# Kernel optimization log

Measured on AMD Instinct MI355X. Metric: run time of the kernel, lower is better.

The kernel has to match this reference:

```python
import jax, jax.numpy as jnp
import numpy as np

TOPK = 8            # args.topk
SWAP_RATIO = 0.3    # args.swap_ratio
NUM_SPECIAL = 999   # first non-special wordpiece id in bert-base-uncased


def setup_inputs() -> dict:
    key = jax.random.key(0)
    k0, k1, k2, k3, k4, k5 = jax.random.split(key, 6)
    B, S, V, D = 4, 512, 30522, 768
    return {
        "delta_grad": jax.random.normal(k0, (B, S, D), jnp.float32),
        "src_embeds": jax.random.normal(k1, (B, S, D), jnp.float32),
        "embedding_matrix": jax.random.normal(k2, (V, D), jnp.float32),
        "src_tokens": jax.random.randint(k3, (B, S), 0, V),
        "pred_lm": jax.random.normal(k4, (B, S, V), jnp.float32),
        "attention_mask": jnp.ones((B, S), jnp.int32),
        "rand_u": jax.random.uniform(k5, (B, S), jnp.float32),
    }


def reference(delta_grad, src_embeds, embedding_matrix, src_tokens, pred_lm, attention_mask, rand_u):
    B, S, D = delta_grad.shape
    V = embedding_matrix.shape[0]
    neg_inf = jnp.float32(-np.inf)

    # dir_dot_grad = -(prev_dot - new_dot) = new_dot - prev_dot
    new_dot = jnp.einsum('bsd,vd->bsv', delta_grad, embedding_matrix)   # [B,S,V]
    prev_dot = jnp.einsum('bsd,bsd->bs', delta_grad, src_embeds)        # [B,S]
    dir_dot_grad = new_dot - prev_dot[..., None]

    # pairwise euclidean distance between src_embeds and vocab embeddings
    src_sq = jnp.sum(src_embeds * src_embeds, axis=-1)                  # [B,S]
    vocab_sq = jnp.sum(embedding_matrix * embedding_matrix, axis=-1)    # [V]
    dot = jnp.einsum('bsd,vd->bsv', src_embeds, embedding_matrix)       # [B,S,V]
    sq_norm = src_sq[..., None] + vocab_sq[None, None, :] - 2.0 * dot
    dir_norm = jnp.sqrt(jax.nn.relu(sq_norm) + 1e-20)

    dir_dot_grad = dir_dot_grad / dir_norm

    # LM top-k allowed-token mask (scatter of 0 into a -inf mask in torch)
    _, topk_idx = jax.lax.top_k(pred_lm, TOPK)                          # [B,S,K]
    topk_idx = topk_idx * attention_mask[..., None].astype(topk_idx.dtype)
    bi = jnp.arange(B)[:, None, None]
    si = jnp.arange(S)[None, :, None]
    allowed = jnp.zeros((B, S, V), bool).at[bi, si, topk_idx].set(True)

    filtered = jnp.where(allowed, dir_dot_grad, neg_inf)
    # special tokens [:999] -> -inf (overrides any topk scatter there)
    filtered = jnp.where(jnp.arange(V)[None, None, :] < NUM_SPECIAL, neg_inf, filtered)
    # forbid keeping the original token
    filtered = jnp.where(jnp.arange(V)[None, None, :] == src_tokens[..., None], neg_inf, filtered)

    adv_flip = jnp.argmax(filtered, axis=2)                             # [B,S]

    # swap mask: non-special positions, Bernoulli(swap_ratio)
    no_special = src_tokens >= NUM_SPECIAL
    swap = rand_u > (1.0 - SWAP_RATIO)
    mask_idx = (no_special & swap).astype(src_tokens.dtype)

    adv_tokens = src_tokens * (1 - mask_idx) + adv_flip.astype(src_tokens.dtype) * mask_idx
    return adv_tokens
```

## Files before the change

### kernel.cpp

```cpp
#include <hip/hip_runtime.h>
#include <math.h>

constexpr int TOPK = 8;
constexpr int NUM_SPECIAL = 999;
constexpr int V = 30522;
constexpr int D = 768;
constexpr int BLOCK = 256;
constexpr int V4 = 7630;
constexpr int NK4 = (V4 + BLOCK - 1) / BLOCK;
constexpr int CAP = 512;
constexpr int HOTCAP = 64;

__device__ __forceinline__ unsigned long long fkey(float v, unsigned int idx) {
    unsigned int u = __float_as_uint(v);
    u = ((int)u < 0) ? ~u : (u | 0x80000000u);
    return ((unsigned long long)u << 32) | (unsigned long long)(~idx);
}

__device__ __forceinline__ void net8(float (&L)[TOPK], float t) {
    #pragma unroll
    for (int j = 0; j < TOPK; ++j) {
        float m = fmaxf(L[j], t); t = fminf(L[j], t); L[j] = m;
    }
}

__device__ __forceinline__ void wave_extract8(float (&cur)[TOPK], int lane,
                                              float* dst) {
    #pragma unroll
    for (int r = 0; r < TOPK; ++r) {
        float m = cur[0];
        int ml = lane;
        #pragma unroll
        for (int off = 1; off < 64; off <<= 1) {
            float om = __shfl_xor(m, off, 64);
            int   ol = __shfl_xor(ml, off, 64);
            if (om > m || (om == m && ol < ml)) { m = om; ml = ol; }
        }
        if (lane == ml) {
            #pragma unroll
            for (int j = 0; j < TOPK - 1; ++j) cur[j] = cur[j + 1];
            cur[TOPK - 1] = -INFINITY;
        }
        if (lane == 0) dst[r] = m;
    }
}

__global__ __launch_bounds__(BLOCK, 8) void dvat_kernel(
    const float* __restrict__ delta_grad,
    const float* __restrict__ src_embeds,
    const float* __restrict__ emb,
    const int*   __restrict__ src_tokens,
    const float* __restrict__ pred_lm,
    const int*   __restrict__ attn,
    const float* __restrict__ rand_u,
    int* __restrict__ out)
{
    const int pos = blockIdx.x;
    const int tid = threadIdx.x;
    const int lane = tid & 63;
    const int wave = tid >> 6;

    __shared__ float  smax[BLOCK];
    __shared__ float  sm8[TOPK];
    __shared__ float  s_g8;
    __shared__ int    s_hot[HOTCAP];
    __shared__ int    s_nhot;
    __shared__ int    s_ncand;
    __shared__ unsigned long long sh_cand64[CAP];
    __shared__ int    s_cand[TOPK];
    __shared__ double s_scores[TOPK];
    __shared__ double s_pd[4], s_ssq[4];
    __shared__ float4 shf4[2 * D / 4];

    if (tid == 0) { s_nhot = 0; s_ncand = 0; }

    const float* rowf = pred_lm + (size_t)pos * V;
    const int ofs = (pos & 1) << 1;
    const float4* row4 = (const float4*)(rowf + ofs);

    float m0 = -INFINITY, m1 = -INFINITY, m2 = -INFINITY, m3 = -INFINITY;
    int i = tid;
    for (int q = 0; q < 7; ++q, i += 4 * BLOCK) {
        float4 a = row4[i];
        float4 b = row4[i + BLOCK];
        float4 c = row4[i + 2 * BLOCK];
        float4 d = row4[i + 3 * BLOCK];
        m0 = fmaxf(m0, fmaxf(fmaxf(a.x, a.y), fmaxf(a.z, a.w)));
        m1 = fmaxf(m1, fmaxf(fmaxf(b.x, b.y), fmaxf(b.z, b.w)));
        m2 = fmaxf(m2, fmaxf(fmaxf(c.x, c.y), fmaxf(c.z, c.w)));
        m3 = fmaxf(m3, fmaxf(fmaxf(d.x, d.y), fmaxf(d.z, d.w)));
    }
    for (; i < V4; i += BLOCK) {
        float4 a = row4[i];
        m0 = fmaxf(m0, fmaxf(fmaxf(a.x, a.y), fmaxf(a.z, a.w)));
    }
    const float tm = fmaxf(fmaxf(m0, m1), fmaxf(m2, m3));
    smax[tid] = tm;
    __syncthreads();

    if (wave == 0) {
        float L[TOPK];
        #pragma unroll
        for (int j = 0; j < TOPK; ++j) L[j] = -INFINITY;
        net8(L, smax[lane]);
        net8(L, smax[lane + 64]);
        net8(L, smax[lane + 128]);
        net8(L, smax[lane + 192]);
        wave_extract8(L, lane, sm8);
        if (lane == 0) s_g8 = sm8[TOPK - 1];
    }
    __syncthreads();
    const float g8 = s_g8;

    if (tm >= g8) {
        int p = atomicAdd(&s_nhot, 1);
        if (p < HOTCAP) s_hot[p] = tid;
    }
    __syncthreads();

    if (tid == 0) {
        #pragma unroll
        for (int e = 0; e < 2; ++e) {
            const int idx = ofs ? e : (V4 * 4 + e);
            const float f = rowf[idx];
            if (f >= g8) {
                int p = atomicAdd(&s_ncand, 1);
                if (p < CAP) sh_cand64[p] = fkey(f, (unsigned)idx);
            }
        }
    }

    if (s_nhot <= HOTCAP) {
        const int nhot = s_nhot;
        const int total = nhot * NK4;
        for (int w = tid; w < total; w += BLOCK) {
            const int h = w / NK4;
            const int k = w - h * NK4;
            const int i4 = s_hot[h] + (k << 8);
            if (i4 < V4) {
                const float4 f = row4[i4];
                const int base = ofs + 4 * i4;
                if (f.x >= g8) { int p = atomicAdd(&s_ncand, 1); if (p < CAP) sh_cand64[p] = fkey(f.x, (unsigned)base); }
                if (f.y >= g8) { int p = atomicAdd(&s_ncand, 1); if (p < CAP) sh_cand64[p] = fkey(f.y, (unsigned)(base + 1)); }
                if (f.z >= g8) { int p = atomicAdd(&s_ncand, 1); if (p < CAP) sh_cand64[p] = fkey(f.z, (unsigned)(base + 2)); }
                if (f.w >= g8) { int p = atomicAdd(&s_ncand, 1); if (p < CAP) sh_cand64[p] = fkey(f.w, (unsigned)(base + 3)); }
            }
        }
    } else {
        for (int i4 = tid; i4 < V4; i4 += BLOCK) {
            const float4 f = row4[i4];
            const int base = ofs + 4 * i4;
            if (f.x >= g8) { int p = atomicAdd(&s_ncand, 1); if (p < CAP) sh_cand64[p] = fkey(f.x, (unsigned)base); }
            if (f.y >= g8) { int p = atomicAdd(&s_ncand, 1); if (p < CAP) sh_cand64[p] = fkey(f.y, (unsigned)(base + 1)); }
            if (f.z >= g8) { int p = atomicAdd(&s_ncand, 1); if (p < CAP) sh_cand64[p] = fkey(f.z, (unsigned)(base + 2)); }
            if (f.w >= g8) { int p = atomicAdd(&s_ncand, 1); if (p < CAP) sh_cand64[p] = fkey(f.w, (unsigned)(base + 3)); }
        }
    }
    __syncthreads();
    const int ncand = min(s_ncand, CAP);

    for (int it = 0; it < TOPK; ++it) {
        if (tid < 64) {
            unsigned long long m = 0ull; int ms = 0;
            for (int j = tid; j < ncand; j += 64) {
                unsigned long long x = sh_cand64[j];
                if (x > m) { m = x; ms = j; }
            }
            #pragma unroll
            for (int off = 32; off; off >>= 1) {
                unsigned long long om = __shfl_down(m, off, 64);
                int os = __shfl_down(ms, off, 64);
                if (om > m) { m = om; ms = os; }
            }
            if (tid == 0) {
                s_cand[it] = (m == 0ull) ? 0 : (int)(~(unsigned int)m);
                sh_cand64[ms] = 0ull;
            }
        }
        __syncthreads();
    }

    if (tid == 0 && attn[pos] == 0) {
        #pragma unroll
        for (int k = 0; k < TOPK; ++k) s_cand[k] = 0;
    }
    __syncthreads();

    const float* dg = delta_grad + (size_t)pos * D;
    const float* se = src_embeds + (size_t)pos * D;

    double pd = 0.0, ssq = 0.0;
    for (int ii = tid; ii < D / 4; ii += BLOCK) {
        const float4 g = ((const float4*)dg)[ii];
        const float4 e = ((const float4*)se)[ii];
        shf4[ii] = g;
        shf4[D / 4 + ii] = e;
        pd  += (double)g.x * (double)e.x + (double)g.y * (double)e.y
             + (double)g.z * (double)e.z + (double)g.w * (double)e.w;
        ssq += (double)e.x * (double)e.x + (double)e.y * (double)e.y
             + (double)e.z * (double)e.z + (double)e.w * (double)e.w;
    }
    #pragma unroll
    for (int off = 32; off; off >>= 1) {
        pd  += __shfl_down(pd, off, 64);
        ssq += __shfl_down(ssq, off, 64);
    }
    if (lane == 0) { s_pd[wave] = pd; s_ssq[wave] = ssq; }
    __syncthreads();

    const double prev_dot = s_pd[0] + s_pd[1] + s_pd[2] + s_pd[3];
    const double src_sq   = s_ssq[0] + s_ssq[1] + s_ssq[2] + s_ssq[3];

    #pragma unroll
    for (int kk = 0; kk < 2; ++kk) {
        const int k = 2 * wave + kk;
        const int v = s_cand[k];
        const float4* ev4 = (const float4*)(emb + (size_t)v * D);
        double ddg = 0.0, dse = 0.0, dvv = 0.0;
        for (int ii = lane; ii < D / 4; ii += 64) {
            const float4 e = ev4[ii];
            const float4 g = shf4[ii];
            const float4 s = shf4[D / 4 + ii];
            ddg += (double)e.x * (double)g.x + (double)e.y * (double)g.y
                 + (double)e.z * (double)g.z + (double)e.w * (double)g.w;
            dse += (double)e.x * (double)s.x + (double)e.y * (double)s.y
                 + (double)e.z * (double)s.z + (double)e.w * (double)s.w;
            dvv += (double)e.x * (double)e.x + (double)e.y * (double)e.y
                 + (double)e.z * (double)e.z + (double)e.w * (double)e.w;
        }
        #pragma unroll
        for (int off = 32; off; off >>= 1) {
            ddg += __shfl_down(ddg, off, 64);
            dse += __shfl_down(dse, off, 64);
            dvv += __shfl_down(dvv, off, 64);
        }
        if (lane == 0) {
            double sq = src_sq + dvv - 2.0 * dse;
            if (sq < 0.0) sq = 0.0;
            double dn = sqrt(sq + 1e-20);
            s_scores[k] = (ddg - prev_dot) / dn;
        }
    }
    __syncthreads();

    if (tid == 0) {
        const int src_tok = src_tokens[pos];
        int best = 0;
        double best_s = 0.0;
        bool found = false;
        #pragma unroll
        for (int k = 0; k < TOPK; ++k) {
            const int v = s_cand[k];
            if (v < NUM_SPECIAL || v == src_tok) continue;
            const double sc = s_scores[k];
            if (!found || sc > best_s || (sc == best_s && v < best)) {
                best = v; best_s = sc; found = true;
            }
        }
        const int adv_flip = found ? best : 0;
        const bool no_special = (src_tok >= NUM_SPECIAL);
        const bool swap = (rand_u[pos] > 0.7f);
        out[pos] = (no_special && swap) ? adv_flip : src_tok;
    }
}

extern "C" void kernel_launch(void* const* d_in, const int* in_sizes, int n_in,
                              void* d_out, int out_size, void* d_ws, size_t ws_size,
                              hipStream_t stream) {
    const float* delta_grad = (const float*)d_in[0];
    const float* src_embeds = (const float*)d_in[1];
    const float* emb        = (const float*)d_in[2];
    const int*   src_tokens = (const int*)d_in[3];
    const float* pred_lm    = (const float*)d_in[4];
    const int*   attn       = (const int*)d_in[5];
    const float* randu      = (const float*)d_in[6];
    int* out = (int*)d_out;

    const int BS = in_sizes[3];
    dvat_kernel<<<BS, BLOCK, 0, stream>>>(delta_grad, src_embeds, emb,
                                          src_tokens, pred_lm, attn, randu, out);
}
```

Baseline: 414.5 us.

## Split top-k and scoring into two kernels; widen max-scan unroll to eight loads

The fused per-position kernel becomes two kernels. The first does the pred_lm top-8 selection and writes the candidate ids to workspace. The second is a single-wave kernel that loads all 8 candidate embedding rows into registers at once and scores them without shared memory or block barriers. The first-pass max scan also goes from 4 to 8 independent float4 loads per iteration, putting more loads in flight. In exchange there is an extra launch, a global round-trip for the candidates, and more register pressure in the scoring kernel.

```diff
diff --git a/kernel.cpp b/kernel.cpp
--- a/kernel.cpp
+++ b/kernel.cpp
@@ -17,6 +17,10 @@
     return ((unsigned long long)u << 32) | (unsigned long long)(~idx);
 }
 
+__device__ __forceinline__ float hmax4(float4 f) {
+    return fmaxf(fmaxf(f.x, f.y), fmaxf(f.z, f.w));
+}
+
 __device__ __forceinline__ void net8(float (&L)[TOPK], float t) {
     #pragma unroll
     for (int j = 0; j < TOPK; ++j) {
@@ -45,15 +49,9 @@
     }
 }
 
-__global__ __launch_bounds__(BLOCK, 8) void dvat_kernel(
-    const float* __restrict__ delta_grad,
-    const float* __restrict__ src_embeds,
-    const float* __restrict__ emb,
-    const int*   __restrict__ src_tokens,
+__global__ __launch_bounds__(BLOCK, 8) void dvat_topk(
     const float* __restrict__ pred_lm,
-    const int*   __restrict__ attn,
-    const float* __restrict__ rand_u,
-    int* __restrict__ out)
+    int* __restrict__ cand_out)
 {
     const int pos = blockIdx.x;
     const int tid = threadIdx.x;
@@ -67,10 +65,6 @@
     __shared__ int    s_nhot;
     __shared__ int    s_ncand;
     __shared__ unsigned long long sh_cand64[CAP];
-    __shared__ int    s_cand[TOPK];
-    __shared__ double s_scores[TOPK];
-    __shared__ double s_pd[4], s_ssq[4];
-    __shared__ float4 shf4[2 * D / 4];
 
     if (tid == 0) { s_nhot = 0; s_ncand = 0; }
 
@@ -78,23 +72,35 @@
     const int ofs = (pos & 1) << 1;
     const float4* row4 = (const float4*)(rowf + ofs);
 
-    float m0 = -INFINITY, m1 = -INFINITY, m2 = -INFINITY, m3 = -INFINITY;
+    float m[8];
+    #pragma unroll
+    for (int j = 0; j < 8; ++j) m[j] = -INFINITY;
+
     int i = tid;
-    for (int q = 0; q < 7; ++q, i += 4 * BLOCK) {
-        float4 a = row4[i];
-        float4 b = row4[i + BLOCK];
-        float4 c = row4[i + 2 * BLOCK];
-        float4 d = row4[i + 3 * BLOCK];
-        m0 = fmaxf(m0, fmaxf(fmaxf(a.x, a.y), fmaxf(a.z, a.w)));
-        m1 = fmaxf(m1, fmaxf(fmaxf(b.x, b.y), fmaxf(b.z, b.w)));
-        m2 = fmaxf(m2, fmaxf(fmaxf(c.x, c.y), fmaxf(c.z, c.w)));
-        m3 = fmaxf(m3, fmaxf(fmaxf(d.x, d.y), fmaxf(d.z, d.w)));
+    for (int q = 0; q < 3; ++q, i += 8 * BLOCK) {
+        float4 f0 = row4[i];
+        float4 f1 = row4[i + BLOCK];
+        float4 f2 = row4[i + 2 * BLOCK];
+        float4 f3 = row4[i + 3 * BLOCK];
+        float4 f4 = row4[i + 4 * BLOCK];
+        float4 f5 = row4[i + 5 * BLOCK];
+        float4 f6 = row4[i + 6 * BLOCK];
+        float4 f7 = row4[i + 7 * BLOCK];
+        m[0] = fmaxf(m[0], hmax4(f0));
+        m[1] = fmaxf(m[1], hmax4(f1));
+        m[2] = fmaxf(m[2], hmax4(f2));
+        m[3] = fmaxf(m[3], hmax4(f3));
+        m[4] = fmaxf(m[4], hmax4(f4));
+        m[5] = fmaxf(m[5], hmax4(f5));
+        m[6] = fmaxf(m[6], hmax4(f6));
+        m[7] = fmaxf(m[7], hmax4(f7));
     }
     for (; i < V4; i += BLOCK) {
-        float4 a = row4[i];
-        m0 = fmaxf(m0, fmaxf(fmaxf(a.x, a.y), fmaxf(a.z, a.w)));
-    }
-    const float tm = fmaxf(fmaxf(m0, m1), fmaxf(m2, m3));
+        float4 f = row4[i];
+        m[0] = fmaxf(m[0], hmax4(f));
+    }
+    const float tm = fmaxf(fmaxf(fmaxf(m[0], m[1]), fmaxf(m[2], m[3])),
+                           fmaxf(fmaxf(m[4], m[5]), fmaxf(m[6], m[7])));
     smax[tid] = tm;
     __syncthreads();
 
@@ -159,68 +165,92 @@
     __syncthreads();
     const int ncand = min(s_ncand, CAP);
 
-    for (int it = 0; it < TOPK; ++it) {
-        if (tid < 64) {
-            unsigned long long m = 0ull; int ms = 0;
-            for (int j = tid; j < ncand; j += 64) {
+    if (wave == 0) {
+        for (int it = 0; it < TOPK; ++it) {
+            unsigned long long mm = 0ull; int ms = 0;
+            for (int j = lane; j < ncand; j += 64) {
                 unsigned long long x = sh_cand64[j];
-                if (x > m) { m = x; ms = j; }
+                if (x > mm) { mm = x; ms = j; }
             }
             #pragma unroll
             for (int off = 32; off; off >>= 1) {
-                unsigned long long om = __shfl_down(m, off, 64);
+                unsigned long long om = __shfl_down(mm, off, 64);
                 int os = __shfl_down(ms, off, 64);
-                if (om > m) { m = om; ms = os; }
-            }
-            if (tid == 0) {
-                s_cand[it] = (m == 0ull) ? 0 : (int)(~(unsigned int)m);
+                if (om > mm) { mm = om; ms = os; }
+            }
+            if (lane == 0) {
+                cand_out[pos * TOPK + it] =
+                    (mm == 0ull) ? 0 : (int)(~(unsigned int)mm);
                 sh_cand64[ms] = 0ull;
             }
         }
-        __syncthreads();
-    }
-
-    if (tid == 0 && attn[pos] == 0) {
-        #pragma unroll
-        for (int k = 0; k < TOPK; ++k) s_cand[k] = 0;
-    }
-    __syncthreads();
-
-    const float* dg = delta_grad + (size_t)pos * D;
-    const float* se = src_embeds + (size_t)pos * D;
+    }
+}
+
+__global__ __launch_bounds__(64) void dvat_score(
+    const float* __restrict__ delta_grad,
+    const float* __restrict__ src_embeds,
+    const float* __restrict__ emb,
+    const int*   __restrict__ src_tokens,
+    const int*   __restrict__ attn,
+    const float* __restrict__ rand_u,
+    const int*   __restrict__ cand_in,
+    int* __restrict__ out)
+{
+    const int pos = blockIdx.x;
+    const int lane = threadIdx.x;
+
+    const bool amask = (attn[pos] != 0);
+    int cand[TOPK];
+    #pragma unroll
+    for (int k = 0; k < TOPK; ++k)
+        cand[k] = amask ? cand_in[pos * TOPK + k] : 0;
+
+    const float4* dg4 = (const float4*)(delta_grad + (size_t)pos * D);
+    const float4* se4 = (const float4*)(src_embeds + (size_t)pos * D);
+    float4 g0 = dg4[lane], g1 = dg4[lane + 64], g2 = dg4[lane + 128];
+    float4 e0 = se4[lane], e1 = se4[lane + 64], e2 = se4[lane + 128];
+
+    float4 q[TOPK][3];
+    #pragma unroll
+    for (int k = 0; k < TOPK; ++k) {
+        const float4* ev4 = (const float4*)(emb + (size_t)cand[k] * D);
+        q[k][0] = ev4[lane];
+        q[k][1] = ev4[lane + 64];
+        q[k][2] = ev4[lane + 128];
+    }
 
     double pd = 0.0, ssq = 0.0;
-    for (int ii = tid; ii < D / 4; ii += BLOCK) {
-        const float4 g = ((const float4*)dg)[ii];
-        const float4 e = ((const float4*)se)[ii];
-        shf4[ii] = g;
-        shf4[D / 4 + ii] = e;
-        pd  += (double)g.x * (double)e.x + (double)g.y * (double)e.y
-             + (double)g.z * (double)e.z + (double)g.w * (double)e.w;
-        ssq += (double)e.x * (double)e.x + (double)e.y * (double)e.y
-             + (double)e.z * (double)e.z + (double)e.w * (double)e.w;
+    {
+        const float4 gs[3] = {g0, g1, g2};
+        const float4 es[3] = {e0, e1, e2};
+        #pragma unroll
+        for (int t = 0; t < 3; ++t) {
+            const float4 g = gs[t], e = es[t];
+            pd  += (double)g.x * (double)e.x + (double)g.y * (double)e.y
+                 + (double)g.z * (double)e.z + (double)g.w * (double)e.w;
+            ssq += (double)e.x * (double)e.x + (double)e.y * (double)e.y
+                 + (double)e.z * (double)e.z + (double)e.w * (double)e.w;
+        }
     }
     #pragma unroll
     for (int off = 32; off; off >>= 1) {
         pd  += __shfl_down(pd, off, 64);
         ssq += __shfl_down(ssq, off, 64);
     }
-    if (lane == 0) { s_pd[wave] = pd; s_ssq[wave] = ssq; }
-    __syncthreads();
-
-    const double prev_dot = s_pd[0] + s_pd[1] + s_pd[2] + s_pd[3];
-    const double src_sq   = s_ssq[0] + s_ssq[1] + s_ssq[2] + s_ssq[3];
-
-    #pragma unroll
-    for (int kk = 0; kk < 2; ++kk) {
-        const int k = 2 * wave + kk;
-        const int v = s_cand[k];
-        const float4* ev4 = (const float4*)(emb + (size_t)v * D);
+
+    int best = 0; double best_s = 0.0; bool found = false;
+    const int src_tok = src_tokens[pos];
+
+    #pragma unroll
+    for (int k = 0; k < TOPK; ++k) {
+        const float4 gs[3] = {g0, g1, g2};
+        const float4 es[3] = {e0, e1, e2};
         double ddg = 0.0, dse = 0.0, dvv = 0.0;
-        for (int ii = lane; ii < D / 4; ii += 64) {
-            const float4 e = ev4[ii];
-            const float4 g = shf4[ii];
-            const float4 s = shf4[D / 4 + ii];
+        #pragma unroll
+        for (int t = 0; t < 3; ++t) {
+            const float4 e = q[k][t];
+            const float4 g = gs[t], s = es[t];
             ddg += (double)e.x * (double)g.x + (double)e.y * (double)g.y
                  + (double)e.z * (double)g.z + (double)e.w * (double)g.w;
             dse += (double)e.x * (double)s.x + (double)e.y * (double)s.y
@@ -235,28 +265,20 @@
             dvv += __shfl_down(dvv, off, 64);
         }
         if (lane == 0) {
-            double sq = src_sq + dvv - 2.0 * dse;
-            if (sq < 0.0) sq = 0.0;
-            double dn = sqrt(sq + 1e-20);
-            s_scores[k] = (ddg - prev_dot) / dn;
-        }
-    }
-    __syncthreads();
-
-    if (tid == 0) {
-        const int src_tok = src_tokens[pos];
-        int best = 0;
-        double best_s = 0.0;
-        bool found = false;
-        #pragma unroll
-        for (int k = 0; k < TOPK; ++k) {
-            const int v = s_cand[k];
-            if (v < NUM_SPECIAL || v == src_tok) continue;
-            const double sc = s_scores[k];
-            if (!found || sc > best_s || (sc == best_s && v < best)) {
-                best = v; best_s = sc; found = true;
-            }
-        }
+            const int v = cand[k];
+            if (v >= NUM_SPECIAL && v != src_tok) {
+                double sq = ssq + dvv - 2.0 * dse;
+                if (sq < 0.0) sq = 0.0;
+                const double dn = sqrt(sq + 1e-20);
+                const double sc = (ddg - pd) / dn;
+                if (!found || sc > best_s || (sc == best_s && v < best)) {
+                    best = v; best_s = sc; found = true;
+                }
+            }
+        }
+    }
+
+    if (lane == 0) {
         const int adv_flip = found ? best : 0;
         const bool no_special = (src_tok >= NUM_SPECIAL);
         const bool swap = (rand_u[pos] > 0.7f);
@@ -277,6 +299,9 @@
     int* out = (int*)d_out;
 
     const int BS = in_sizes[3];
-    dvat_kernel<<<BS, BLOCK, 0, stream>>>(delta_grad, src_embeds, emb,
-                                          src_tokens, pred_lm, attn, randu, out);
-}
+    int* cand_ws = (int*)d_ws;
+
+    dvat_topk<<<BS, BLOCK, 0, stream>>>(pred_lm, cand_ws);
+    dvat_score<<<BS, 64, 0, stream>>>(delta_grad, src_embeds, emb,
+                                      src_tokens, attn, randu, cand_ws, out);
+}
```

Result: no change. 414.8 us (+0.1%).
